# Kernel tuning notes

Hardware: AMD Instinct MI355X
Metric: run time of the kernel (lower is better)

Reference implementation:

```python
import jax, jax.numpy as jnp
import numpy as np

N_NODES = 50000
N_EDGES = 800000
IN_C, HID_C, OUT_C, HEADS = 128, 32, 64, 8
NEG_SLOPE = 0.2


def gat_layer(x, src, dst, W, a_src, a_dst, bias, concat, num_nodes):
    # W: [F_in, H*C]; a_src, a_dst: [H, C]; bias: [H*C] or [C]
    H, C = a_src.shape
    h = (x @ W).reshape(num_nodes, H, C)                      # [N,H,C]
    e_src = (h * a_src).sum(-1)                               # [N,H]
    e_dst = (h * a_dst).sum(-1)                               # [N,H]
    e = jax.nn.leaky_relu(e_src[src] + e_dst[dst], NEG_SLOPE) # [E,H]
    # segment softmax over incoming edges of each destination node
    m = jax.ops.segment_max(e, dst, num_segments=num_nodes)   # [N,H]
    ex = jnp.exp(e - m[dst])
    den = jax.ops.segment_sum(ex, dst, num_segments=num_nodes)
    alpha = ex / (den[dst] + 1e-16)                           # [E,H]
    out = jax.ops.segment_sum(h[src] * alpha[..., None], dst, num_segments=num_nodes)  # [N,H,C]
    out = out.reshape(num_nodes, H * C) if concat else out.mean(axis=1)
    return out + bias


def setup_inputs() -> dict:
    key = jax.random.key(0)
    ks = jax.random.split(key, 10)
    x = jax.random.normal(ks[0], (N_NODES, IN_C), dtype=jnp.float32)
    edge_index = jax.random.randint(ks[1], (2, N_EDGES), 0, N_NODES, dtype=jnp.int64)
    s1 = (2.0 / (IN_C + HID_C * HEADS)) ** 0.5
    s2 = (2.0 / (HID_C * HEADS + OUT_C)) ** 0.5
    return {
        "x": x,
        "edge_index": edge_index,
        "W1": jax.random.normal(ks[2], (IN_C, HEADS * HID_C), dtype=jnp.float32) * s1,
        "a_src1": jax.random.normal(ks[3], (HEADS, HID_C), dtype=jnp.float32) * 0.1,
        "a_dst1": jax.random.normal(ks[4], (HEADS, HID_C), dtype=jnp.float32) * 0.1,
        "b1": jnp.zeros((HEADS * HID_C,), dtype=jnp.float32),
        "W2": jax.random.normal(ks[5], (HEADS * HID_C, OUT_C), dtype=jnp.float32) * s2,
        "a_src2": jax.random.normal(ks[6], (1, OUT_C), dtype=jnp.float32) * 0.1,
        "a_dst2": jax.random.normal(ks[7], (1, OUT_C), dtype=jnp.float32) * 0.1,
        "b2": jnp.zeros((OUT_C,), dtype=jnp.float32),
    }


def reference(x, edge_index, W1, a_src1, a_dst1, b1, W2, a_src2, a_dst2, b2):
    # add self-loops (PyG GATConv default)
    loops = jnp.arange(N_NODES, dtype=edge_index.dtype)
    src = jnp.concatenate([edge_index[0], loops])
    dst = jnp.concatenate([edge_index[1], loops])
    # dropout layers are identity in eval mode
    h = gat_layer(x, src, dst, W1, a_src1, a_dst1, b1, True, N_NODES)
    h = jax.nn.elu(h)
    out = gat_layer(h, src, dst, W2, a_src2, a_dst2, b2, False, N_NODES)
    return out
```

## Files before the change

kernel.cpp:

```cpp
#include <hip/hip_runtime.h>
#include <math.h>

#define N_NODES 50000
#define N_EDGES 800000
#define E_TOT   850000
#define IN_C    128
#define HID_C   32
#define OUT_C   64
#define HEADS   8
#define F1      256
#define PAD     64
#define NDUMMY  1024
#define G1_BLOCKS 3125
#define CSR_BLOCKS 782

typedef __bf16 bf16x8 __attribute__((ext_vector_type(8)));
typedef float  f32x4  __attribute__((ext_vector_type(4)));
typedef float  f32x2  __attribute__((ext_vector_type(2)));
typedef unsigned short us8 __attribute__((ext_vector_type(8)));

__device__ __forceinline__ unsigned short f2b(float f) {
    unsigned u = __float_as_uint(f);
    u += 0x7FFF + ((u >> 16) & 1);
    return (unsigned short)(u >> 16);
}
__device__ __forceinline__ float b2f(unsigned short b) {
    return __uint_as_float(((unsigned)b) << 16);
}
__device__ __forceinline__ float blo(unsigned u) { return __uint_as_float(u << 16); }
__device__ __forceinline__ float bhi(unsigned u) { return __uint_as_float(u & 0xffff0000u); }
__device__ __forceinline__ f32x2 up2(unsigned u) {
    f32x2 r; r.x = blo(u); r.y = bhi(u); return r;
}

__global__ void convert_w(const float* __restrict__ W1, const float* __restrict__ W2,
                          unsigned short* __restrict__ W1t, unsigned short* __restrict__ W2t,
                          int* __restrict__ deg, int* __restrict__ ssrc) {
    int gid = blockIdx.x * 256 + threadIdx.x;
    if (gid < N_NODES) {
        deg[gid] = 1;
        ssrc[gid * PAD] = gid;
    } else if (gid < N_NODES + NDUMMY) {
        deg[gid] = 0;
    }
    if (gid < 256 * 128) {
        int n = gid >> 7, k = gid & 127;
        W1t[gid] = f2b(W1[k * F1 + n]);
    } else if (gid < 256 * 128 + 64 * 256) {
        int o = gid - 256 * 128;
        int n = o >> 8, k = o & 255;
        W2t[o] = f2b(W2[k * OUT_C + n]);
    }
}

__global__ void csr_build(const int* __restrict__ ei, int* __restrict__ deg,
                          int* __restrict__ ssrc) {
    int e0 = blockIdx.x * 1024 + threadIdx.x;
    int s[4], d[4], p[4];
#pragma unroll
    for (int j = 0; j < 4; j++) {
        int e = e0 + j * 256;
        int le = (e < N_EDGES) ? e : (N_EDGES - 1);
        int es = ei[le];
        int ed = ei[N_EDGES + le];
        s[j] = es;
        d[j] = (e < N_EDGES) ? ed : (N_NODES + (e - N_EDGES));
    }
#pragma unroll
    for (int j = 0; j < 4; j++) p[j] = atomicAdd(&deg[d[j]], 1);
#pragma unroll
    for (int j = 0; j < 4; j++) ssrc[d[j] * PAD + p[j]] = s[j];
}

__global__ __launch_bounds__(256) void gemm1_mfma(const float* __restrict__ x,
                                                  const unsigned short* __restrict__ W1t,
                                                  const float* __restrict__ a_src,
                                                  const float* __restrict__ a_dst,
                                                  unsigned short* __restrict__ h1b,
                                                  float* __restrict__ e_src,
                                                  float* __restrict__ e_dst) {
    const int t = threadIdx.x;
    const int wave = t >> 6, lane = t & 63;
    const int mlane = lane & 15, quad = lane >> 4;
    const int row0 = blockIdx.x * 16;
    const int col0 = wave * 64;
    const float* xr = x + (size_t)(row0 + mlane) * IN_C;
    bf16x8 afr[4];
#pragma unroll
    for (int kc = 0; kc < 4; kc++) {
        float4 f0 = *(const float4*)&xr[kc * 32 + quad * 8];
        float4 f1 = *(const float4*)&xr[kc * 32 + quad * 8 + 4];
        us8 u;
        u[0] = f2b(f0.x); u[1] = f2b(f0.y); u[2] = f2b(f0.z); u[3] = f2b(f0.w);
        u[4] = f2b(f1.x); u[5] = f2b(f1.y); u[6] = f2b(f1.z); u[7] = f2b(f1.w);
        afr[kc] = __builtin_bit_cast(bf16x8, u);
    }
    f32x4 c[4];
#pragma unroll
    for (int nt = 0; nt < 4; nt++) c[nt] = (f32x4){0.f, 0.f, 0.f, 0.f};
#pragma unroll
    for (int kc = 0; kc < 4; kc++) {
#pragma unroll
        for (int nt = 0; nt < 4; nt++) {
            int col = col0 + nt * 16 + mlane;
            uint4 bw = *(const uint4*)&W1t[(size_t)col * IN_C + kc * 32 + quad * 8];
            bf16x8 b = __builtin_bit_cast(bf16x8, bw);
            c[nt] = __builtin_amdgcn_mfma_f32_16x16x32_bf16(afr[kc], b, c[nt], 0, 0, 0);
        }
    }
#pragma unroll
    for (int nt = 0; nt < 4; nt++) {
#pragma unroll
        for (int r = 0; r < 4; r++) {
            int gr = row0 + quad * 4 + r;
            h1b[(size_t)gr * F1 + col0 + nt * 16 + mlane] = f2b(c[nt][r]);
        }
    }
    float asA0 = a_src[col0 + mlane],      asA1 = a_src[col0 + 16 + mlane];
    float asB0 = a_src[col0 + 32 + mlane], asB1 = a_src[col0 + 48 + mlane];
    float adA0 = a_dst[col0 + mlane],      adA1 = a_dst[col0 + 16 + mlane];
    float adB0 = a_dst[col0 + 32 + mlane], adB1 = a_dst[col0 + 48 + mlane];
#pragma unroll
    for (int r = 0; r < 4; r++) {
        float psA = c[0][r] * asA0 + c[1][r] * asA1;
        float pdA = c[0][r] * adA0 + c[1][r] * adA1;
        float psB = c[2][r] * asB0 + c[3][r] * asB1;
        float pdB = c[2][r] * adB0 + c[3][r] * adB1;
#pragma unroll
        for (int off = 1; off < 16; off <<= 1) {
            psA += __shfl_xor(psA, off, 64);
            pdA += __shfl_xor(pdA, off, 64);
            psB += __shfl_xor(psB, off, 64);
            pdB += __shfl_xor(pdB, off, 64);
        }
        if (mlane == 0) {
            int gr = row0 + quad * 4 + r;
            e_src[gr * HEADS + wave * 2]     = psA;
            e_src[gr * HEADS + wave * 2 + 1] = psB;
            e_dst[gr * HEADS + wave * 2]     = pdA;
            e_dst[gr * HEADS + wave * 2 + 1] = pdB;
        }
    }
}

__global__ __launch_bounds__(256) void agg1s(const unsigned short* __restrict__ h1b,
                                             const float* __restrict__ e_src,
                                             const float* __restrict__ e_dst,
                                             const int* __restrict__ deg,
                                             const int* __restrict__ ssrc,
                                             const float* __restrict__ b1,
                                             unsigned short* __restrict__ hhb) {
    int v = (blockIdx.x * 256 + threadIdx.x) >> 6;
    if (v >= N_NODES) return;
    int lane = threadIdx.x & 63;
    int half = lane >> 5, l32 = lane & 31;
    int c0 = l32 * 8, h_acc = l32 >> 2;
    int c2 = c0 << 1;
    int h_exp = l32 & 7;
    int j_exp = l32 >> 3;
    const char* h1c = (const char*)h1b;
    const char* esc = (const char*)e_src;
    int d = deg[v];
    int beg = v * PAD;
    int s_all = ssrc[beg + lane];
    float edh_x = e_dst[v * HEADS + h_exp];
    float edh_a = e_dst[v * HEADS + h_acc];
    f32x2 acc[4];
#pragma unroll
    for (int k = 0; k < 4; k++) acc[k] = (f32x2){0.f, 0.f};
    float den = 0.f;
    int k8 = 0;
    for (; k8 + 7 < d; k8 += 8) {
        int slot_e = k8 + half + 2 * j_exp;
        int s_e = __shfl(s_all, slot_e, 64);
        float e = *(const float*)(esc + ((s_e << 5) + (h_exp << 2))) + edh_x;
        e = fmaxf(e, 0.2f * e);
        float w = __expf(e);
        int b0 = k8 + half;
        int s0 = __shfl(s_all, b0,     64);
        int s1 = __shfl(s_all, b0 + 2, 64);
        int s2 = __shfl(s_all, b0 + 4, 64);
        int s3 = __shfl(s_all, b0 + 6, 64);
        float w0 = __shfl(w, (0 << 3) | h_acc, 32);
        float w1 = __shfl(w, (1 << 3) | h_acc, 32);
        float w2 = __shfl(w, (2 << 3) | h_acc, 32);
        float w3 = __shfl(w, (3 << 3) | h_acc, 32);
        den += (w0 + w1) + (w2 + w3);
        uint4 r0 = *(const uint4*)(h1c + ((s0 << 9) + c2));
        uint4 r1 = *(const uint4*)(h1c + ((s1 << 9) + c2));
        uint4 r2 = *(const uint4*)(h1c + ((s2 << 9) + c2));
        uint4 r3 = *(const uint4*)(h1c + ((s3 << 9) + c2));
        acc[0] += w0 * up2(r0.x) + w1 * up2(r1.x) + w2 * up2(r2.x) + w3 * up2(r3.x);
        acc[1] += w0 * up2(r0.y) + w1 * up2(r1.y) + w2 * up2(r2.y) + w3 * up2(r3.y);
        acc[2] += w0 * up2(r0.z) + w1 * up2(r1.z) + w2 * up2(r2.z) + w3 * up2(r3.z);
        acc[3] += w0 * up2(r0.w) + w1 * up2(r1.w) + w2 * up2(r2.w) + w3 * up2(r3.w);
    }
    int i = beg + k8 + half, end = beg + d;
    for (; i < end; i += 2) {
        int s0 = ssrc[i];
        float e0 = *(const float*)(esc + ((s0 << 5) + (h_acc << 2))) + edh_a;
        e0 = fmaxf(e0, 0.2f * e0);
        float w0 = __expf(e0);
        den += w0;
        uint4 r0 = *(const uint4*)(h1c + ((s0 << 9) + c2));
        acc[0] += w0 * up2(r0.x);
        acc[1] += w0 * up2(r0.y);
        acc[2] += w0 * up2(r0.z);
        acc[3] += w0 * up2(r0.w);
    }
    den += __shfl_xor(den, 32, 64);
#pragma unroll
    for (int k = 0; k < 4; k++) {
        acc[k].x += __shfl_xor(acc[k].x, 32, 64);
        acc[k].y += __shfl_xor(acc[k].y, 32, 64);
    }
    if (half == 0) {
        float dinv = 1.f / (den + 1e-16f);
        us8 o;
#pragma unroll
        for (int k = 0; k < 4; k++) {
            float v0 = acc[k].x * dinv + b1[c0 + 2 * k];
            float v1 = acc[k].y * dinv + b1[c0 + 2 * k + 1];
            v0 = (v0 > 0.f) ? v0 : expm1f(v0);
            v1 = (v1 > 0.f) ? v1 : expm1f(v1);
            o[2 * k]     = f2b(v0);
            o[2 * k + 1] = f2b(v1);
        }
        *(us8*)&hhb[(size_t)v * F1 + c0] = o;
    }
}

__global__ __launch_bounds__(256) void gemm2_mfma(const unsigned short* __restrict__ hhb,
                                                  const unsigned short* __restrict__ W2t,
                                                  const float* __restrict__ a_src,
                                                  const float* __restrict__ a_dst,
                                                  unsigned short* __restrict__ h2b,
                                                  float* __restrict__ e_src,
                                                  float* __restrict__ e_dst) {
    const int t = threadIdx.x;
    const int wave = t >> 6, lane = t & 63;
    const int mlane = lane & 15, quad = lane >> 4;
    const int row0 = blockIdx.x * 64 + wave * 16;
    int arow = row0 + mlane;
    if (arow >= N_NODES) arow = N_NODES - 1;
    const unsigned short* ar = hhb + (size_t)arow * F1;
    f32x4 c[4];
#pragma unroll
    for (int nt = 0; nt < 4; nt++) c[nt] = (f32x4){0.f, 0.f, 0.f, 0.f};
#pragma unroll
    for (int kc = 0; kc < 8; kc++) {
        uint4 aw = *(const uint4*)&ar[kc * 32 + quad * 8];
        bf16x8 a = __builtin_bit_cast(bf16x8, aw);
#pragma unroll
        for (int nt = 0; nt < 4; nt++) {
            int col = nt * 16 + mlane;
            uint4 bw = *(const uint4*)&W2t[(size_t)col * F1 + kc * 32 + quad * 8];
            bf16x8 b = __builtin_bit_cast(bf16x8, bw);
            c[nt] = __builtin_amdgcn_mfma_f32_16x16x32_bf16(a, b, c[nt], 0, 0, 0);
        }
    }
#pragma unroll
    for (int nt = 0; nt < 4; nt++) {
#pragma unroll
        for (int r = 0; r < 4; r++) {
            int gr = row0 + quad * 4 + r;
            if (gr < N_NODES)
                h2b[(size_t)gr * OUT_C + nt * 16 + mlane] = f2b(c[nt][r]);
        }
    }
    float as0 = a_src[mlane],      as1 = a_src[16 + mlane];
    float as2 = a_src[32 + mlane], as3 = a_src[48 + mlane];
    float ad0 = a_dst[mlane],      ad1 = a_dst[16 + mlane];
    float ad2 = a_dst[32 + mlane], ad3 = a_dst[48 + mlane];
#pragma unroll
    for (int r = 0; r < 4; r++) {
        float ps = c[0][r] * as0 + c[1][r] * as1 + c[2][r] * as2 + c[3][r] * as3;
        float pd = c[0][r] * ad0 + c[1][r] * ad1 + c[2][r] * ad2 + c[3][r] * ad3;
#pragma unroll
        for (int off = 1; off < 16; off <<= 1) {
            ps += __shfl_xor(ps, off, 64);
            pd += __shfl_xor(pd, off, 64);
        }
        int gr = row0 + quad * 4 + r;
        if (mlane == 0 && gr < N_NODES) { e_src[gr] = ps; e_dst[gr] = pd; }
    }
}

__global__ __launch_bounds__(256) void agg2s(const unsigned short* __restrict__ h2b,
                                             const float* __restrict__ e_src,
                                             const float* __restrict__ e_dst,
                                             const int* __restrict__ deg,
                                             const int* __restrict__ ssrc,
                                             const float* __restrict__ b2,
                                             float* __restrict__ out) {
    int v = (blockIdx.x * 256 + threadIdx.x) >> 6;
    if (v >= N_NODES) return;
    int lane = threadIdx.x & 63;
    int d = deg[v];
    int beg = v * PAD;
    float ed = e_dst[v];
    int g = lane >> 3, l8 = lane & 7;
    int c0 = l8 * 8;
    int c2 = c0 << 1;
    const char* h2c = (const char*)h2b;
    const char* esc = (const char*)e_src;
    int s_all = ssrc[beg + lane];
    f32x2 acc[4];
#pragma unroll
    for (int k = 0; k < 4; k++) acc[k] = (f32x2){0.f, 0.f};
    float den = 0.f;
    for (int k8 = 0; k8 < d; k8 += 8) {
        int slot = k8 + g;
        int s = __shfl(s_all, slot, 64);
        if (slot < d) {
            float e = *(const float*)(esc + (s << 2)) + ed;
            e = fmaxf(e, 0.2f * e);
            float wv = __expf(e);
            den += wv;
            uint4 r = *(const uint4*)(h2c + ((s << 7) + c2));
            acc[0] += wv * up2(r.x);
            acc[1] += wv * up2(r.y);
            acc[2] += wv * up2(r.z);
            acc[3] += wv * up2(r.w);
        }
    }
    den += __shfl_xor(den, 8, 64);
    den += __shfl_xor(den, 16, 64);
    den += __shfl_xor(den, 32, 64);
#pragma unroll
    for (int k = 0; k < 4; k++) {
        acc[k].x += __shfl_xor(acc[k].x, 8, 64);
        acc[k].y += __shfl_xor(acc[k].y, 8, 64);
        acc[k].x += __shfl_xor(acc[k].x, 16, 64);
        acc[k].y += __shfl_xor(acc[k].y, 16, 64);
        acc[k].x += __shfl_xor(acc[k].x, 32, 64);
        acc[k].y += __shfl_xor(acc[k].y, 32, 64);
    }
    if (g == 0) {
        float dinv = 1.f / (den + 1e-16f);
        float4 lo, hi;
        lo.x = acc[0].x * dinv + b2[c0 + 0]; lo.y = acc[0].y * dinv + b2[c0 + 1];
        lo.z = acc[1].x * dinv + b2[c0 + 2]; lo.w = acc[1].y * dinv + b2[c0 + 3];
        hi.x = acc[2].x * dinv + b2[c0 + 4]; hi.y = acc[2].y * dinv + b2[c0 + 5];
        hi.z = acc[3].x * dinv + b2[c0 + 6]; hi.w = acc[3].y * dinv + b2[c0 + 7];
        *(float4*)&out[(size_t)v * OUT_C + c0] = lo;
        *(float4*)&out[(size_t)v * OUT_C + c0 + 4] = hi;
    }
}

extern "C" void kernel_launch(void* const* d_in, const int* in_sizes, int n_in,
                              void* d_out, int out_size, void* d_ws, size_t ws_size,
                              hipStream_t stream) {
    const float* x      = (const float*)d_in[0];
    const int*   ei     = (const int*)d_in[1];
    const float* W1     = (const float*)d_in[2];
    const float* a_src1 = (const float*)d_in[3];
    const float* a_dst1 = (const float*)d_in[4];
    const float* b1     = (const float*)d_in[5];
    const float* W2     = (const float*)d_in[6];
    const float* a_src2 = (const float*)d_in[7];
    const float* a_dst2 = (const float*)d_in[8];
    const float* b2     = (const float*)d_in[9];
    float* out = (float*)d_out;

    char* ws = (char*)d_ws;
    size_t off = 0;
    auto alloc = [&](size_t bytes) { void* p = ws + off; off = (off + bytes + 255) & ~(size_t)255; return p; };
    unsigned short* h1b = (unsigned short*)alloc((size_t)N_NODES * F1 * 2);
    unsigned short* hhb = (unsigned short*)alloc((size_t)N_NODES * F1 * 2);
    unsigned short* h2b = (unsigned short*)alloc((size_t)N_NODES * OUT_C * 2);
    unsigned short* W1t = (unsigned short*)alloc((size_t)256 * 128 * 2);
    unsigned short* W2t = (unsigned short*)alloc((size_t)64 * 256 * 2);
    float* e_src1 = (float*)alloc((size_t)N_NODES * HEADS * 4);
    float* e_dst1 = (float*)alloc((size_t)N_NODES * HEADS * 4);
    float* e_src2 = (float*)alloc((size_t)N_NODES * 4);
    float* e_dst2 = (float*)alloc((size_t)N_NODES * 4);
    int*   deg    = (int*)alloc((size_t)(N_NODES + NDUMMY) * 4);
    int*   ssrc   = (int*)alloc((size_t)(N_NODES + NDUMMY) * PAD * 4);
    (void)ws_size; (void)n_in; (void)in_sizes; (void)out_size;

    const int g2_blocks  = (N_NODES + 63) / 64;
    const int node_waves = (N_NODES + 3) / 4;

    convert_w<<<200, 256, 0, stream>>>(W1, W2, W1t, W2t, deg, ssrc);
    csr_build<<<CSR_BLOCKS, 256, 0, stream>>>(ei, deg, ssrc);
    gemm1_mfma<<<G1_BLOCKS, 256, 0, stream>>>(x, W1t, a_src1, a_dst1, h1b, e_src1, e_dst1);
    agg1s<<<node_waves, 256, 0, stream>>>(h1b, e_src1, e_dst1, deg, ssrc, b1, hhb);
    gemm2_mfma<<<g2_blocks, 256, 0, stream>>>(hhb, W2t, a_src2, a_dst2, h2b, e_src2, e_dst2);
    agg2s<<<node_waves, 256, 0, stream>>>(h2b, e_src2, e_dst2, deg, ssrc, b2, out);
}
```

Before: 295.2 us.

## Store layer-1 features head-major and aggregate one head per block

gemm1 now writes the hidden features in a head-major layout ([head][node][32]) and e_src transposed to [head][node]. agg1s becomes one block per (node group, head), with each wave handling a node for one head and lanes splitting into 16 edges by 4 channel groups. The aim is to shrink each node's gather working set per pass so the per-head feature table (about 3.2MB) stays cache-resident, and to spread the edge loop across more lanes. The cost is eight times as many blocks, eight reads of deg, ssrc and the index loads, a longer shuffle reduction, and smaller 64-byte gathered rows.

Result: slower. 406.2 us (+37.6%).

```diff
diff --git a/kernel.cpp b/kernel.cpp
--- a/kernel.cpp
+++ b/kernel.cpp
@@ -76,8 +76,8 @@
                                                   const unsigned short* __restrict__ W1t,
                                                   const float* __restrict__ a_src,
                                                   const float* __restrict__ a_dst,
-                                                  unsigned short* __restrict__ h1b,
-                                                  float* __restrict__ e_src,
+                                                  unsigned short* __restrict__ h1h,
+                                                  float* __restrict__ e_srcT,
                                                   float* __restrict__ e_dst) {
     const int t = threadIdx.x;
     const int wave = t >> 6, lane = t & 63;
@@ -110,10 +110,12 @@
     }
 #pragma unroll
     for (int nt = 0; nt < 4; nt++) {
+        int hh = wave * 2 + (nt >> 1);
+        int cc = ((nt & 1) << 4) + mlane;
 #pragma unroll
         for (int r = 0; r < 4; r++) {
             int gr = row0 + quad * 4 + r;
-            h1b[(size_t)gr * F1 + col0 + nt * 16 + mlane] = f2b(c[nt][r]);
+            h1h[(size_t)hh * (N_NODES * 32) + (size_t)gr * 32 + cc] = f2b(c[nt][r]);
         }
     }
     float asA0 = a_src[col0 + mlane],      asA1 = a_src[col0 + 16 + mlane];
@@ -135,96 +137,80 @@
         }
         if (mlane == 0) {
             int gr = row0 + quad * 4 + r;
-            e_src[gr * HEADS + wave * 2]     = psA;
-            e_src[gr * HEADS + wave * 2 + 1] = psB;
+            e_srcT[(wave * 2) * N_NODES + gr]     = psA;
+            e_srcT[(wave * 2 + 1) * N_NODES + gr] = psB;
             e_dst[gr * HEADS + wave * 2]     = pdA;
             e_dst[gr * HEADS + wave * 2 + 1] = pdB;
         }
     }
 }
 
-__global__ __launch_bounds__(256) void agg1s(const unsigned short* __restrict__ h1b,
-                                             const float* __restrict__ e_src,
+__global__ __launch_bounds__(256) void agg1s(const unsigned short* __restrict__ h1h,
+                                             const float* __restrict__ e_srcT,
                                              const float* __restrict__ e_dst,
                                              const int* __restrict__ deg,
                                              const int* __restrict__ ssrc,
                                              const float* __restrict__ b1,
                                              unsigned short* __restrict__ hhb) {
-    int v = (blockIdx.x * 256 + threadIdx.x) >> 6;
-    if (v >= N_NODES) return;
-    int lane = threadIdx.x & 63;
-    int half = lane >> 5, l32 = lane & 31;
-    int c0 = l32 * 8, h_acc = l32 >> 2;
-    int c2 = c0 << 1;
-    int h_exp = l32 & 7;
-    int j_exp = l32 >> 3;
-    const char* h1c = (const char*)h1b;
-    const char* esc = (const char*)e_src;
-    int d = deg[v];
-    int beg = v * PAD;
-    int s_all = ssrc[beg + lane];
-    float edh_x = e_dst[v * HEADS + h_exp];
-    float edh_a = e_dst[v * HEADS + h_acc];
+    const int bid = blockIdx.x;
+    const int h = bid & 7;
+    const int wave = threadIdx.x >> 6;
+    const int v = (bid >> 3) * 4 + wave;
+    const int lane = threadIdx.x & 63;
+    const int e16 = lane >> 2, cg = lane & 3;
+    const char* h1c = (const char*)h1h + (size_t)h * (N_NODES * 64);
+    const char* esc = (const char*)e_srcT + (size_t)h * (N_NODES * 4);
+    const int d = deg[v];
+    const int beg = v * PAD;
+    const float edh = e_dst[v * HEADS + h];
+    const int cg16 = cg << 4;
     f32x2 acc[4];
 #pragma unroll
     for (int k = 0; k < 4; k++) acc[k] = (f32x2){0.f, 0.f};
     float den = 0.f;
-    int k8 = 0;
-    for (; k8 + 7 < d; k8 += 8) {
-        int slot_e = k8 + half + 2 * j_exp;
-        int s_e = __shfl(s_all, slot_e, 64);
-        float e = *(const float*)(esc + ((s_e << 5) + (h_exp << 2))) + edh_x;
-        e = fmaxf(e, 0.2f * e);
-        float w = __expf(e);
-        int b0 = k8 + half;
-        int s0 = __shfl(s_all, b0,     64);
-        int s1 = __shfl(s_all, b0 + 2, 64);
-        int s2 = __shfl(s_all, b0 + 4, 64);
-        int s3 = __shfl(s_all, b0 + 6, 64);
-        float w0 = __shfl(w, (0 << 3) | h_acc, 32);
-        float w1 = __shfl(w, (1 << 3) | h_acc, 32);
-        float w2 = __shfl(w, (2 << 3) | h_acc, 32);
-        float w3 = __shfl(w, (3 << 3) | h_acc, 32);
-        den += (w0 + w1) + (w2 + w3);
-        uint4 r0 = *(const uint4*)(h1c + ((s0 << 9) + c2));
-        uint4 r1 = *(const uint4*)(h1c + ((s1 << 9) + c2));
-        uint4 r2 = *(const uint4*)(h1c + ((s2 << 9) + c2));
-        uint4 r3 = *(const uint4*)(h1c + ((s3 << 9) + c2));
-        acc[0] += w0 * up2(r0.x) + w1 * up2(r1.x) + w2 * up2(r2.x) + w3 * up2(r3.x);
-        acc[1] += w0 * up2(r0.y) + w1 * up2(r1.y) + w2 * up2(r2.y) + w3 * up2(r3.y);
-        acc[2] += w0 * up2(r0.z) + w1 * up2(r1.z) + w2 * up2(r2.z) + w3 * up2(r3.z);
-        acc[3] += w0 * up2(r0.w) + w1 * up2(r1.w) + w2 * up2(r2.w) + w3 * up2(r3.w);
-    }
-    int i = beg + k8 + half, end = beg + d;
-    for (; i < end; i += 2) {
-        int s0 = ssrc[i];
-        float e0 = *(const float*)(esc + ((s0 << 5) + (h_acc << 2))) + edh_a;
-        e0 = fmaxf(e0, 0.2f * e0);
-        float w0 = __expf(e0);
-        den += w0;
-        uint4 r0 = *(const uint4*)(h1c + ((s0 << 9) + c2));
-        acc[0] += w0 * up2(r0.x);
-        acc[1] += w0 * up2(r0.y);
-        acc[2] += w0 * up2(r0.z);
-        acc[3] += w0 * up2(r0.w);
-    }
-    den += __shfl_xor(den, 32, 64);
-#pragma unroll
-    for (int k = 0; k < 4; k++) {
-        acc[k].x += __shfl_xor(acc[k].x, 32, 64);
-        acc[k].y += __shfl_xor(acc[k].y, 32, 64);
-    }
-    if (half == 0) {
+    for (int k16 = 0; k16 < d; k16 += 16) {
+        int slot = k16 + e16;
+        if (slot < d) {
+            int s = ssrc[beg + slot];
+            float e = *(const float*)(esc + (s << 2)) + edh;
+            e = fmaxf(e, 0.2f * e);
+            float w = __expf(e);
+            den += w;
+            uint4 r = *(const uint4*)(h1c + ((s << 6) + cg16));
+            acc[0] += w * up2(r.x);
+            acc[1] += w * up2(r.y);
+            acc[2] += w * up2(r.z);
+            acc[3] += w * up2(r.w);
+        }
+    }
+#pragma unroll
+    for (int off = 4; off <= 32; off <<= 1) {
+        den += __shfl_xor(den, off, 64);
+        acc[0].x += __shfl_xor(acc[0].x, off, 64);
+        acc[0].y += __shfl_xor(acc[0].y, off, 64);
+        acc[1].x += __shfl_xor(acc[1].x, off, 64);
+        acc[1].y += __shfl_xor(acc[1].y, off, 64);
+        acc[2].x += __shfl_xor(acc[2].x, off, 64);
+        acc[2].y += __shfl_xor(acc[2].y, off, 64);
+        acc[3].x += __shfl_xor(acc[3].x, off, 64);
+        acc[3].y += __shfl_xor(acc[3].y, off, 64);
+    }
+    if (e16 == 0) {
         float dinv = 1.f / (den + 1e-16f);
+        int c0 = h * 32 + cg * 8;
+        float4 bl = *(const float4*)&b1[c0];
+        float4 bh = *(const float4*)&b1[c0 + 4];
+        float vv[8];
+        vv[0] = acc[0].x * dinv + bl.x; vv[1] = acc[0].y * dinv + bl.y;
+        vv[2] = acc[1].x * dinv + bl.z; vv[3] = acc[1].y * dinv + bl.w;
+        vv[4] = acc[2].x * dinv + bh.x; vv[5] = acc[2].y * dinv + bh.y;
+        vv[6] = acc[3].x * dinv + bh.z; vv[7] = acc[3].y * dinv + bh.w;
         us8 o;
 #pragma unroll
-        for (int k = 0; k < 4; k++) {
-            float v0 = acc[k].x * dinv + b1[c0 + 2 * k];
-            float v1 = acc[k].y * dinv + b1[c0 + 2 * k + 1];
-            v0 = (v0 > 0.f) ? v0 : expm1f(v0);
-            v1 = (v1 > 0.f) ? v1 : expm1f(v1);
-            o[2 * k]     = f2b(v0);
-            o[2 * k + 1] = f2b(v1);
+        for (int k = 0; k < 8; k++) {
+            float y = vv[k];
+            y = (y > 0.f) ? y : expm1f(y);
+            o[k] = f2b(y);
         }
         *(us8*)&hhb[(size_t)v * F1 + c0] = o;
     }
@@ -366,12 +352,12 @@
     char* ws = (char*)d_ws;
     size_t off = 0;
     auto alloc = [&](size_t bytes) { void* p = ws + off; off = (off + bytes + 255) & ~(size_t)255; return p; };
-    unsigned short* h1b = (unsigned short*)alloc((size_t)N_NODES * F1 * 2);
+    unsigned short* h1h = (unsigned short*)alloc((size_t)N_NODES * F1 * 2);
     unsigned short* hhb = (unsigned short*)alloc((size_t)N_NODES * F1 * 2);
     unsigned short* h2b = (unsigned short*)alloc((size_t)N_NODES * OUT_C * 2);
     unsigned short* W1t = (unsigned short*)alloc((size_t)256 * 128 * 2);
     unsigned short* W2t = (unsigned short*)alloc((size_t)64 * 256 * 2);
-    float* e_src1 = (float*)alloc((size_t)N_NODES * HEADS * 4);
+    float* e_srcT = (float*)alloc((size_t)N_NODES * HEADS * 4);
     float* e_dst1 = (float*)alloc((size_t)N_NODES * HEADS * 4);
     float* e_src2 = (float*)alloc((size_t)N_NODES * 4);
     float* e_dst2 = (float*)alloc((size_t)N_NODES * 4);
@@ -381,11 +367,12 @@
 
     const int g2_blocks  = (N_NODES + 63) / 64;
     const int node_waves = (N_NODES + 3) / 4;
+    const int agg1_blocks = (N_NODES / 4) * 8;
 
     convert_w<<<200, 256, 0, stream>>>(W1, W2, W1t, W2t, deg, ssrc);
     csr_build<<<CSR_BLOCKS, 256, 0, stream>>>(ei, deg, ssrc);
-    gemm1_mfma<<<G1_BLOCKS, 256, 0, stream>>>(x, W1t, a_src1, a_dst1, h1b, e_src1, e_dst1);
-    agg1s<<<node_waves, 256, 0, stream>>>(h1b, e_src1, e_dst1, deg, ssrc, b1, hhb);
+    gemm1_mfma<<<G1_BLOCKS, 256, 0, stream>>>(x, W1t, a_src1, a_dst1, h1h, e_srcT, e_dst1);
+    agg1s<<<agg1_blocks, 256, 0, stream>>>(h1h, e_srcT, e_dst1, deg, ssrc, b1, hhb);
     gemm2_mfma<<<g2_blocks, 256, 0, stream>>>(hhb, W2t, a_src2, a_dst2, h2b, e_src2, e_dst2);
     agg2s<<<node_waves, 256, 0, stream>>>(h2b, e_src2, e_dst2, deg, ssrc, b2, out);
 }
```
